# Optimization experiments

Measured on AMD Instinct MI355X. Metric: run time of the kernel, lower is better.

## Reference

```python
import jax, jax.numpy as jnp
import numpy as np

B, T, H, N_CLASSES = 2048, 128, 64, 32
N_STEPS = 10  # euler micro-steps over t in [0,1], step_size=0.1


def setup_inputs() -> dict:
    key = jax.random.key(0)
    ks = jax.random.split(key, 16)
    s = lambda fan_in: 1.0 / np.sqrt(fan_in)
    inp = {
        "times": jax.random.uniform(ks[0], (B, T), jnp.float32),
        "marks": jax.random.randint(ks[1], (B, T, 1), 0, N_CLASSES),
        "mask": jnp.ones((B, T), jnp.float32),
        # Diffeq.net: MLP(H+1 -> H -> H -> H), Tanh activations, Tanh final
        "W0": jax.random.uniform(ks[2], (H, H + 1), jnp.float32, -s(H + 1), s(H + 1)),
        "b0": jax.random.uniform(ks[3], (H,), jnp.float32, -s(H + 1), s(H + 1)),
        "W1": jax.random.uniform(ks[4], (H, H), jnp.float32, -s(H), s(H)),
        "b1": jax.random.uniform(ks[5], (H,), jnp.float32, -s(H), s(H)),
        "W2": jax.random.uniform(ks[6], (H, H), jnp.float32, -s(H), s(H)),
        "b2": jax.random.uniform(ks[7], (H,), jnp.float32, -s(H), s(H)),
        # Diffeq.intensity: Linear(H -> 1) + Softplus
        "Wi": jax.random.uniform(ks[8], (1, H), jnp.float32, -s(H), s(H)),
        "bi": jax.random.uniform(ks[9], (1,), jnp.float32, -s(H), s(H)) + 0.5,
        # Embedding(n_classes, H)
        "emb": jax.random.normal(ks[10], (N_CLASSES, H), jnp.float32),
        # LSTMCell(1+H, H)
        "W_ih": jax.random.uniform(ks[11], (4 * H, 1 + H), jnp.float32, -s(H), s(H)),
        "W_hh": jax.random.uniform(ks[12], (4 * H, H), jnp.float32, -s(H), s(H)),
        "b_ih": jax.random.uniform(ks[13], (4 * H,), jnp.float32, -s(H), s(H)),
        "b_hh": jax.random.uniform(ks[14], (4 * H,), jnp.float32, -s(H), s(H)),
    }
    return inp


def reference(times, marks, mask, W0, b0, W1, b1, W2, b2, Wi, bi, emb,
              W_ih, W_hh, b_ih, b_hh):
    dt = jnp.float32(1.0 / N_STEPS)

    def mlp(x):  # Diffeq.net
        x = jnp.tanh(x @ W0.T + b0)
        x = jnp.tanh(x @ W1.T + b1)
        return jnp.tanh(x @ W2.T + b2)

    def intensity(h):  # Diffeq.intensity (Softplus head) -> (B,1)
        return jax.nn.softplus(h @ Wi.T + bi)

    # faithful to original: marks[:, 1] is used at every timestep
    m1 = emb[marks[:, 1, 0]]  # (B,H)

    def step(carry, t_col):
        h, c = carry                       # (B,H), (B,H)
        t = t_col[:, None]                 # (B,1) -- diff (event time)
        # fixed-step euler solve of the Diffeq over s in [0,1]
        def euler(state, s):
            hh, integ = state
            s_t = (s * dt) * t             # (B,1) integration time scaled
            d_h = mlp(jnp.concatenate([s_t, hh], -1)) * t
            d_i = intensity(hh) * t
            return (hh + dt * d_h, integ + dt * d_i), None
        (h_ode, integ), _ = jax.lax.scan(
            euler, (h, jnp.zeros_like(t)),
            jnp.arange(N_STEPS, dtype=times.dtype))
        inten = intensity(h_ode)           # (B,1)
        # LSTMCell update with input [t, mark_embedding]
        x_in = jnp.concatenate([t, m1], -1)           # (B,1+H)
        gates = x_in @ W_ih.T + b_ih + h_ode @ W_hh.T + b_hh
        i_g, f_g, g_g, o_g = jnp.split(gates, 4, -1)
        c_new = jax.nn.sigmoid(f_g) * c + jax.nn.sigmoid(i_g) * jnp.tanh(g_g)
        h_new = jax.nn.sigmoid(o_g) * jnp.tanh(c_new)
        nll = (-jnp.log(inten) + integ)[:, 0]          # (B,)
        return (h_new, c_new), (h_ode, nll)

    h0 = jnp.zeros((times.shape[0], emb.shape[1]), times.dtype)
    _, (hidden, nll) = jax.lax.scan(step, (h0, h0), times.T)
    hidden = jnp.transpose(hidden, (1, 0, 2))   # (B,T,H)
    nll = nll.T                                  # (B,T)
    loss = (nll * mask).sum() / mask.sum()
    return loss, hidden
```

## Files before the change

### kernel.cpp

```cpp
#include <hip/hip_runtime.h>


#define T_LEN 128

typedef float  f32x4  __attribute__((ext_vector_type(4)));
typedef __bf16 bf16x8 __attribute__((ext_vector_type(8)));
typedef __bf16 bf16x2 __attribute__((ext_vector_type(2)));

#define MFMA16(a, b, c) __builtin_amdgcn_mfma_f32_16x16x32_bf16((a), (b), (c), 0, 0, 0)

__device__ __forceinline__ float rcp_f(float x) { return __builtin_amdgcn_rcpf(x); }
__device__ __forceinline__ float exp2_f(float x) { return __builtin_amdgcn_exp2f(x); }
__device__ __forceinline__ float log2_f(float x) { return __builtin_amdgcn_logf(x); }

__device__ __forceinline__ void bar_lds() {
  asm volatile("s_waitcnt lgkmcnt(0)" ::: "memory");
  __builtin_amdgcn_s_barrier();
  __builtin_amdgcn_sched_barrier(0);
}

constexpr float kL2E = 1.44269504088896340736f;
constexpr float kLN2 = 0.69314718055994530942f;

__device__ __forceinline__ float tanh_fast(float x) {
  float e = exp2_f(x * (2.0f * kL2E));
  return 1.0f - 2.0f * rcp_f(e + 1.0f);
}
__device__ __forceinline__ float sigm_fast(float x) {
  return rcp_f(1.0f + exp2_f(-kL2E * x));
}
__device__ __forceinline__ float softplus_fast(float x) {
  float neg = log2_f(1.0f + exp2_f(-kL2E * fabsf(x))) * kLN2;
  return fmaxf(x, 0.0f) + neg;
}
__device__ __forceinline__ unsigned packbf(float a, float b) {
  bf16x2 v; v[0] = (__bf16)a; v[1] = (__bf16)b;
  return __builtin_bit_cast(unsigned, v);
}

__launch_bounds__(256)
__global__ void jumpode_main(
    const float* __restrict__ times, const int* __restrict__ marks,
    const float* __restrict__ maskp, const float* __restrict__ W0,
    const float* __restrict__ b0,    const float* __restrict__ W1,
    const float* __restrict__ b1,    const float* __restrict__ W2,
    const float* __restrict__ b2,    const float* __restrict__ Wi,
    const float* __restrict__ bi,    const float* __restrict__ emb,
    const float* __restrict__ W_ih,  const float* __restrict__ W_hh,
    const float* __restrict__ b_ih,  const float* __restrict__ b_hh,
    float* __restrict__ out, float* __restrict__ ws)
{
  __shared__ __align__(16) unsigned whh_l[256 * 32];
  __shared__ __align__(16) float    gm1_l[8 * 256];
  __shared__ __align__(16) unsigned xb0[16 * 32];
  __shared__ __align__(16) unsigned xb1[16 * 32];
  __shared__ __align__(16) unsigned xb2[16 * 32];
  __shared__ __align__(16) float    pint[3][160];
  __shared__ __align__(16) float    b0_l[64], b1_l[64], b2_l[64];
  __shared__ __align__(16) float    w0c0_l[64];
  __shared__ __align__(16) float    wihc0_l[256];
  __shared__ __align__(16) float    emb16[8][64];
  __shared__ __align__(16) float    tim_l[8][T_LEN];
  __shared__ __align__(16) float    msk_l[8][T_LEN];

  const int tid = threadIdx.x;
  const int wv  = tid >> 6;
  const int l   = tid & 63;
  const int b   = l & 15;
  const int q   = l >> 4;
  const int bm  = b & 7;
  const int row = blockIdx.x * 8 + bm;
  const int xsw = bm;

  if (tid < 64) {
    b0_l[tid] = b0[tid]; b1_l[tid] = b1[tid]; b2_l[tid] = b2[tid];
    w0c0_l[tid] = W0[tid * 65];
  }
  wihc0_l[tid] = W_ih[tid * 65];
  for (int idx = tid; idx < 512; idx += 256) {
    int rr = idx >> 6, cc = idx & 63;
    int mk = marks[(blockIdx.x * 8 + rr) * T_LEN + 1];
    emb16[rr][cc] = emb[mk * 64 + cc];
  }
  for (int idx = tid; idx < 1024; idx += 256) {
    int rr = idx >> 7, cc = idx & 127;
    tim_l[rr][cc] = times[(blockIdx.x * 8 + rr) * T_LEN + cc];
    msk_l[rr][cc] = maskp[(blockIdx.x * 8 + rr) * T_LEN + cc];
  }
  #pragma unroll 4
  for (int i = 0; i < 32; ++i) {
    int idx = i * 256 + tid;
    int rw = idx >> 5, c2 = idx & 31;
    unsigned pw = packbf(W_hh[rw * 64 + 2 * c2], W_hh[rw * 64 + 2 * c2 + 1]);
    int gr = c2 >> 2;
    whh_l[rw * 32 + ((gr ^ (rw & 7)) << 2) + (c2 & 3)] = pw;
  }
  __syncthreads();

  {
    int g = tid;
    float acc[8];
    #pragma unroll
    for (int bb = 0; bb < 8; ++bb) acc[bb] = 0.0f;
    const float* wr = &W_ih[g * 65 + 1];
    for (int k = 0; k < 64; ++k) {
      float w = wr[k];
      #pragma unroll
      for (int bb = 0; bb < 8; ++bb) acc[bb] += w * emb16[bb][k];
    }
    float bias = b_ih[g] + b_hh[g];
    int gg = g >> 2;
    #pragma unroll
    for (int bb = 0; bb < 8; ++bb)
      gm1_l[bb * 256 + ((gg ^ bb) << 2) + (g & 3)] = acc[bb] + bias;
  }

  bf16x8 w0f[2], w1f[2], w2f[2];
  {
    const int fm = 16 * wv + b;
    #pragma unroll
    for (int kt = 0; kt < 2; ++kt) {
      const float* r0 = &W0[fm * 65 + 1 + kt * 32 + q * 8];
      const float* r1 = &W1[fm * 64 +     kt * 32 + q * 8];
      const float* r2 = &W2[fm * 64 +     kt * 32 + q * 8];
      bf16x8 a, bb, c;
      #pragma unroll
      for (int e = 0; e < 8; ++e) {
        a[e] = (__bf16)r0[e]; bb[e] = (__bf16)r1[e]; c[e] = (__bf16)r2[e];
      }
      w0f[kt] = a; w1f[kt] = bb; w2f[kt] = c;
    }
  }
  f32x4 wiv;
  #pragma unroll
  for (int r = 0; r < 4; ++r) wiv[r] = Wi[16 * wv + 4 * q + r];
  const float bi_s = bi[0];
  const f32x4 b0v = *(const f32x4*)&b0_l[16 * wv + 4 * q];
  const f32x4 b1v = *(const f32x4*)&b1_l[16 * wv + 4 * q];
  const f32x4 b2v = *(const f32x4*)&b2_l[16 * wv + 4 * q];
  const f32x4 c0v = *(const f32x4*)&w0c0_l[16 * wv + 4 * q];
  const f32x4 zf  = (f32x4){0.f, 0.f, 0.f, 0.f};
  __syncthreads();

  auto write_x = [&](unsigned* buf, const f32x4 v) {
    if (b < 8) {
      int gr = (2 * wv + (q >> 1)) ^ xsw;
      int wb = b * 32 + (gr << 2) + ((q & 1) << 1);
      buf[wb]     = packbf(v[0], v[1]);
      buf[wb + 1] = packbf(v[2], v[3]);
    }
  };
  auto read_bfrag = [&](const unsigned* buf, int kt) -> bf16x8 {
    int gr = (kt * 4 + q) ^ xsw;
    return *(const bf16x8*)((const char*)buf + bm * 128 + gr * 16);
  };
  auto whh_frag = [&](int R, int kt) -> bf16x8 {
    int rw = R * 16 + b;
    int gr = (kt * 4 + q) ^ (b & 7);
    return *(const bf16x8*)((const char*)whh_l + rw * 128 + gr * 16);
  };
  auto ld_gm1 = [&](int R) -> f32x4 {
    int gr = (R * 4 + q) ^ bm;
    return *(const f32x4*)((const char*)gm1_l + bm * 1024 + gr * 16);
  };
  auto isect_partial = [&](float* pb, const f32x4 v) {
    float part = wiv[0] * v[0] + wiv[1] * v[1] + wiv[2] * v[2] + wiv[3] * v[3];
    if (b < 8) pb[b * 20 + wv * 4 + q] = part;
  };
  auto isect_sum = [&](const float* pb) -> float {
    const char* base = (const char*)pb + bm * 80;
    f32x4 p0 = *(const f32x4*)(base);
    f32x4 p1 = *(const f32x4*)(base + 16);
    f32x4 p2 = *(const f32x4*)(base + 32);
    f32x4 p3 = *(const f32x4*)(base + 48);
    f32x4 s = p0 + p1 + p2 + p3;
    return s[0] + s[1] + s[2] + s[3];
  };

  f32x4 hst = zf, cst = zf;
  float nll_acc = 0.f, m_acc = 0.f;
  const float sel0 = (wv == 0 && q == 0 && b < 8) ? 1.0f : 0.0f;

  f32x4 hh, cin1;
  float integ, dtt, st, tb;

  auto euler_substep = [&](unsigned* BA, unsigned* BB, float* PB) {
    isect_partial(PB, hh);
    write_x(BA, hh);
    bar_lds();
    bf16x8 Bf0 = read_bfrag(BA, 0), Bf1 = read_bfrag(BA, 1);

    f32x4 a0 = MFMA16(w0f[0], Bf0, cin1);
    f32x4 a1 = MFMA16(w0f[1], Bf1, zf);
    integ += dtt * softplus_fast(isect_sum(PB) + bi_s);
    f32x4 y;
    #pragma unroll
    for (int r = 0; r < 4; ++r) y[r] = tanh_fast(a0[r] + a1[r]);
    write_x(BB, y);
    bar_lds();
    Bf0 = read_bfrag(BB, 0); Bf1 = read_bfrag(BB, 1);

    a0 = MFMA16(w1f[0], Bf0, b1v);
    a1 = MFMA16(w1f[1], Bf1, zf);
    #pragma unroll
    for (int r = 0; r < 4; ++r) y[r] = tanh_fast(a0[r] + a1[r]);
    write_x(BA, y);
    bar_lds();
    Bf0 = read_bfrag(BA, 0); Bf1 = read_bfrag(BA, 1);

    a0 = MFMA16(w2f[0], Bf0, b2v);
    a1 = MFMA16(w2f[1], Bf1, zf);
    st += dtt;
    #pragma unroll
    for (int r = 0; r < 4; ++r) cin1[r] = b0v[r] + c0v[r] * st;
    #pragma unroll
    for (int r = 0; r < 4; ++r) hh[r] += dtt * tanh_fast(a0[r] + a1[r]);
  };

  #pragma unroll 1
  for (int step = 0; step < T_LEN; ++step) {
    tb  = tim_l[bm][step];
    dtt = 0.1f * tb;
    hh  = hst;
    integ = 0.f;
    st  = 0.f;
    cin1 = b0v;

    f32x4 gcin[4];
    #pragma unroll
    for (int g = 0; g < 4; ++g) {
      const int Rb = 4 * g + wv;
      f32x4 gm = ld_gm1(Rb);
      f32x4 wc = *(const f32x4*)&wihc0_l[Rb * 16 + q * 4];
      #pragma unroll
      for (int r = 0; r < 4; ++r) gcin[g][r] = gm[r] + wc[r] * tb;
    }

    #pragma unroll 1
    for (int s2 = 0; s2 < 5; ++s2) {
      euler_substep(xb0, xb1, pint[0]);
      euler_substep(xb1, xb0, pint[1]);
    }

    bf16x8 wf[4][2];
    #pragma unroll
    for (int g = 0; g < 4; ++g) {
      wf[g][0] = whh_frag(4 * g + wv, 0);
      wf[g][1] = whh_frag(4 * g + wv, 1);
    }
    isect_partial(pint[2], hh);
    write_x(xb2, hh);
    if (b < 8) {
      size_t obase = 1 + (((size_t)row) * T_LEN + step) * 64 + 16 * wv + 4 * q;
      out[obase + 0] = hh[0]; out[obase + 1] = hh[1];
      out[obase + 2] = hh[2]; out[obase + 3] = hh[3];
    }
    bar_lds();
    bf16x8 Bf0 = read_bfrag(xb2, 0), Bf1 = read_bfrag(xb2, 1);

    f32x4 ga[4];
    #pragma unroll
    for (int g = 0; g < 4; ++g) {
      f32x4 a = MFMA16(wf[g][0], Bf0, gcin[g]);
      ga[g] = MFMA16(wf[g][1], Bf1, a);
    }
    {
      float inten = softplus_fast(isect_sum(pint[2]) + bi_s);
      float nll = -(log2_f(inten) * kLN2) + integ;
      float mval = msk_l[bm][step];
      nll_acc += sel0 * mval * nll;
      m_acc   += sel0 * mval;
    }
    #pragma unroll
    for (int r = 0; r < 4; ++r) {
      float ig = sigm_fast(ga[0][r]), fg = sigm_fast(ga[1][r]);
      float gg = tanh_fast(ga[2][r]), og = sigm_fast(ga[3][r]);
      float cn = fg * cst[r] + ig * gg;
      cst[r] = cn;
      hst[r] = og * tanh_fast(cn);
    }
  }

  if (wv == 0) {
    #pragma unroll
    for (int off = 1; off < 64; off <<= 1) {
      nll_acc += __shfl_xor(nll_acc, off);
      m_acc   += __shfl_xor(m_acc, off);
    }
    if (tid == 0) {
      atomicAdd(&ws[0], nll_acc);
      atomicAdd(&ws[1], m_acc);
    }
  }
}

__global__ void jumpode_fin(const float* __restrict__ ws, float* __restrict__ out) {
  if (threadIdx.x == 0 && blockIdx.x == 0) out[0] = ws[0] / ws[1];
}

extern "C" void kernel_launch(void* const* d_in, const int* in_sizes, int n_in,
                              void* d_out, int out_size, void* d_ws, size_t ws_size,
                              hipStream_t stream) {
  (void)in_sizes; (void)n_in; (void)out_size; (void)ws_size;
  const float* times = (const float*)d_in[0];
  const int*   marks = (const int*)  d_in[1];
  const float* maskp = (const float*)d_in[2];
  const float* W0    = (const float*)d_in[3];
  const float* b0    = (const float*)d_in[4];
  const float* W1    = (const float*)d_in[5];
  const float* b1    = (const float*)d_in[6];
  const float* W2    = (const float*)d_in[7];
  const float* b2    = (const float*)d_in[8];
  const float* Wi    = (const float*)d_in[9];
  const float* bi    = (const float*)d_in[10];
  const float* emb   = (const float*)d_in[11];
  const float* W_ih  = (const float*)d_in[12];
  const float* W_hh  = (const float*)d_in[13];
  const float* b_ih  = (const float*)d_in[14];
  const float* b_hh  = (const float*)d_in[15];
  float* out = (float*)d_out;
  float* ws  = (float*)d_ws;

  (void)hipMemsetAsync(d_ws, 0, 2 * sizeof(float), stream);
  jumpode_main<<<dim3(256), dim3(256), 0, stream>>>(
      times, marks, maskp, W0, b0, W1, b1, W2, b2, Wi, bi, emb,
      W_ih, W_hh, b_ih, b_hh, out, ws);
  jumpode_fin<<<dim3(1), dim3(64), 0, stream>>>(ws, out);
}
```

Before: 909.8 us.

## Process two independent row chains per block and halve the grid

```diff
diff --git a/kernel.cpp b/kernel.cpp
--- a/kernel.cpp
+++ b/kernel.cpp
@@ -51,17 +51,17 @@
     float* __restrict__ out, float* __restrict__ ws)
 {
   __shared__ __align__(16) unsigned whh_l[256 * 32];
-  __shared__ __align__(16) float    gm1_l[8 * 256];
+  __shared__ __align__(16) float    gm1_l[16 * 256];
   __shared__ __align__(16) unsigned xb0[16 * 32];
   __shared__ __align__(16) unsigned xb1[16 * 32];
   __shared__ __align__(16) unsigned xb2[16 * 32];
-  __shared__ __align__(16) float    pint[3][160];
+  __shared__ __align__(16) float    pint[3][320];
   __shared__ __align__(16) float    b0_l[64], b1_l[64], b2_l[64];
   __shared__ __align__(16) float    w0c0_l[64];
   __shared__ __align__(16) float    wihc0_l[256];
-  __shared__ __align__(16) float    emb16[8][64];
-  __shared__ __align__(16) float    tim_l[8][T_LEN];
-  __shared__ __align__(16) float    msk_l[8][T_LEN];
+  __shared__ __align__(16) float    emb16[16][64];
+  __shared__ __align__(16) float    tim_l[16][T_LEN];
+  __shared__ __align__(16) float    msk_l[16][T_LEN];
 
   const int tid = threadIdx.x;
   const int wv  = tid >> 6;
@@ -69,23 +69,22 @@
   const int b   = l & 15;
   const int q   = l >> 4;
   const int bm  = b & 7;
-  const int row = blockIdx.x * 8 + bm;
-  const int xsw = bm;
+  const int rowbase = blockIdx.x * 16;
 
   if (tid < 64) {
     b0_l[tid] = b0[tid]; b1_l[tid] = b1[tid]; b2_l[tid] = b2[tid];
     w0c0_l[tid] = W0[tid * 65];
   }
   wihc0_l[tid] = W_ih[tid * 65];
-  for (int idx = tid; idx < 512; idx += 256) {
+  for (int idx = tid; idx < 1024; idx += 256) {
     int rr = idx >> 6, cc = idx & 63;
-    int mk = marks[(blockIdx.x * 8 + rr) * T_LEN + 1];
+    int mk = marks[(rowbase + rr) * T_LEN + 1];
     emb16[rr][cc] = emb[mk * 64 + cc];
   }
-  for (int idx = tid; idx < 1024; idx += 256) {
+  for (int idx = tid; idx < 2048; idx += 256) {
     int rr = idx >> 7, cc = idx & 127;
-    tim_l[rr][cc] = times[(blockIdx.x * 8 + rr) * T_LEN + cc];
-    msk_l[rr][cc] = maskp[(blockIdx.x * 8 + rr) * T_LEN + cc];
+    tim_l[rr][cc] = times[(rowbase + rr) * T_LEN + cc];
+    msk_l[rr][cc] = maskp[(rowbase + rr) * T_LEN + cc];
   }
   #pragma unroll 4
   for (int i = 0; i < 32; ++i) {
@@ -99,20 +98,20 @@
 
   {
     int g = tid;
-    float acc[8];
-    #pragma unroll
-    for (int bb = 0; bb < 8; ++bb) acc[bb] = 0.0f;
+    float acc[16];
+    #pragma unroll
+    for (int bb = 0; bb < 16; ++bb) acc[bb] = 0.0f;
     const float* wr = &W_ih[g * 65 + 1];
     for (int k = 0; k < 64; ++k) {
       float w = wr[k];
       #pragma unroll
-      for (int bb = 0; bb < 8; ++bb) acc[bb] += w * emb16[bb][k];
+      for (int bb = 0; bb < 16; ++bb) acc[bb] += w * emb16[bb][k];
     }
     float bias = b_ih[g] + b_hh[g];
     int gg = g >> 2;
     #pragma unroll
-    for (int bb = 0; bb < 8; ++bb)
-      gm1_l[bb * 256 + ((gg ^ bb) << 2) + (g & 3)] = acc[bb] + bias;
+    for (int bb = 0; bb < 16; ++bb)
+      gm1_l[bb * 256 + ((gg ^ (bb & 7)) << 2) + (g & 3)] = acc[bb] + bias;
   }
 
   bf16x8 w0f[2], w1f[2], w2f[2];
@@ -142,33 +141,38 @@
   const f32x4 zf  = (f32x4){0.f, 0.f, 0.f, 0.f};
   __syncthreads();
 
-  auto write_x = [&](unsigned* buf, const f32x4 v) {
-    if (b < 8) {
-      int gr = (2 * wv + (q >> 1)) ^ xsw;
-      int wb = b * 32 + (gr << 2) + ((q & 1) << 1);
-      buf[wb]     = packbf(v[0], v[1]);
-      buf[wb + 1] = packbf(v[2], v[3]);
-    }
-  };
-  auto read_bfrag = [&](const unsigned* buf, int kt) -> bf16x8 {
-    int gr = (kt * 4 + q) ^ xsw;
-    return *(const bf16x8*)((const char*)buf + bm * 128 + gr * 16);
+  auto write_x = [&](unsigned* buf, const f32x4 vA, const f32x4 vB) {
+    f32x4 v;
+    #pragma unroll
+    for (int r = 0; r < 4; ++r) v[r] = (b < 8) ? vA[r] : vB[r];
+    int gr = (2 * wv + (q >> 1)) ^ bm;
+    int wb = b * 32 + (gr << 2) + ((q & 1) << 1);
+    buf[wb]     = packbf(v[0], v[1]);
+    buf[wb + 1] = packbf(v[2], v[3]);
+  };
+  auto read_bfrag = [&](const unsigned* buf, int kt, int chain) -> bf16x8 {
+    int col = bm + 8 * chain;
+    int gr = (kt * 4 + q) ^ bm;
+    return *(const bf16x8*)((const char*)buf + col * 128 + gr * 16);
   };
   auto whh_frag = [&](int R, int kt) -> bf16x8 {
     int rw = R * 16 + b;
     int gr = (kt * 4 + q) ^ (b & 7);
     return *(const bf16x8*)((const char*)whh_l + rw * 128 + gr * 16);
   };
-  auto ld_gm1 = [&](int R) -> f32x4 {
-    int gr = (R * 4 + q) ^ bm;
-    return *(const f32x4*)((const char*)gm1_l + bm * 1024 + gr * 16);
-  };
-  auto isect_partial = [&](float* pb, const f32x4 v) {
+  auto ld_gm1 = [&](int row, int R) -> f32x4 {
+    int gr = (R * 4 + q) ^ (row & 7);
+    return *(const f32x4*)((const char*)gm1_l + row * 1024 + gr * 16);
+  };
+  auto isect_partial = [&](float* pb, const f32x4 vA, const f32x4 vB) {
+    f32x4 v;
+    #pragma unroll
+    for (int r = 0; r < 4; ++r) v[r] = (b < 8) ? vA[r] : vB[r];
     float part = wiv[0] * v[0] + wiv[1] * v[1] + wiv[2] * v[2] + wiv[3] * v[3];
-    if (b < 8) pb[b * 20 + wv * 4 + q] = part;
+    pb[b * 20 + wv * 4 + q] = part;
   };
   auto isect_sum = [&](const float* pb) -> float {
-    const char* base = (const char*)pb + bm * 80;
+    const char* base = (const char*)pb + b * 80;
     f32x4 p0 = *(const f32x4*)(base);
     f32x4 p1 = *(const f32x4*)(base + 16);
     f32x4 p2 = *(const f32x4*)(base + 32);
@@ -177,64 +181,77 @@
     return s[0] + s[1] + s[2] + s[3];
   };
 
-  f32x4 hst = zf, cst = zf;
+  f32x4 hstA = zf, cstA = zf, hstB = zf, cstB = zf;
   float nll_acc = 0.f, m_acc = 0.f;
-  const float sel0 = (wv == 0 && q == 0 && b < 8) ? 1.0f : 0.0f;
-
-  f32x4 hh, cin1;
-  float integ, dtt, st, tb;
+  const float sel = (wv == 0 && q == 0) ? 1.0f : 0.0f;
+
+  f32x4 hhA, hhB, cin1A, cin1B;
+  float integ_own, dttA, dttB, dtt_own, stA, stB, tbA, tbB;
 
   auto euler_substep = [&](unsigned* BA, unsigned* BB, float* PB) {
-    isect_partial(PB, hh);
-    write_x(BA, hh);
+    isect_partial(PB, hhA, hhB);
+    write_x(BA, hhA, hhB);
     bar_lds();
-    bf16x8 Bf0 = read_bfrag(BA, 0), Bf1 = read_bfrag(BA, 1);
-
-    f32x4 a0 = MFMA16(w0f[0], Bf0, cin1);
-    f32x4 a1 = MFMA16(w0f[1], Bf1, zf);
-    integ += dtt * softplus_fast(isect_sum(PB) + bi_s);
-    f32x4 y;
-    #pragma unroll
-    for (int r = 0; r < 4; ++r) y[r] = tanh_fast(a0[r] + a1[r]);
-    write_x(BB, y);
+    bf16x8 A0 = read_bfrag(BA, 0, 0), A1 = read_bfrag(BA, 1, 0);
+    bf16x8 B0 = read_bfrag(BA, 0, 1), B1 = read_bfrag(BA, 1, 1);
+
+    f32x4 aA0 = MFMA16(w0f[0], A0, cin1A);
+    f32x4 aA1 = MFMA16(w0f[1], A1, zf);
+    f32x4 aB0 = MFMA16(w0f[0], B0, cin1B);
+    f32x4 aB1 = MFMA16(w0f[1], B1, zf);
+    integ_own += dtt_own * softplus_fast(isect_sum(PB) + bi_s);
+    f32x4 yA, yB;
+    #pragma unroll
+    for (int r = 0; r < 4; ++r) {
+      yA[r] = tanh_fast(aA0[r] + aA1[r]);
+      yB[r] = tanh_fast(aB0[r] + aB1[r]);
+    }
+    write_x(BB, yA, yB);
     bar_lds();
-    Bf0 = read_bfrag(BB, 0); Bf1 = read_bfrag(BB, 1);
-
-    a0 = MFMA16(w1f[0], Bf0, b1v);
-    a1 = MFMA16(w1f[1], Bf1, zf);
-    #pragma unroll
-    for (int r = 0; r < 4; ++r) y[r] = tanh_fast(a0[r] + a1[r]);
-    write_x(BA, y);
+    A0 = read_bfrag(BB, 0, 0); A1 = read_bfrag(BB, 1, 0);
+    B0 = read_bfrag(BB, 0, 1); B1 = read_bfrag(BB, 1, 1);
+
+    aA0 = MFMA16(w1f[0], A0, b1v);
+    aA1 = MFMA16(w1f[1], A1, zf);
+    aB0 = MFMA16(w1f[0], B0, b1v);
+    aB1 = MFMA16(w1f[1], B1, zf);
+    #pragma unroll
+    for (int r = 0; r < 4; ++r) {
+      yA[r] = tanh_fast(aA0[r] + aA1[r]);
+      yB[r] = tanh_fast(aB0[r] + aB1[r]);
+    }
+    write_x(BA, yA, yB);
     bar_lds();
-    Bf0 = read_bfrag(BA, 0); Bf1 = read_bfrag(BA, 1);
-
-    a0 = MFMA16(w2f[0], Bf0, b2v);
-    a1 = MFMA16(w2f[1], Bf1, zf);
-    st += dtt;
-    #pragma unroll
-    for (int r = 0; r < 4; ++r) cin1[r] = b0v[r] + c0v[r] * st;
-    #pragma unroll
-    for (int r = 0; r < 4; ++r) hh[r] += dtt * tanh_fast(a0[r] + a1[r]);
+    A0 = read_bfrag(BA, 0, 0); A1 = read_bfrag(BA, 1, 0);
+    B0 = read_bfrag(BA, 0, 1); B1 = read_bfrag(BA, 1, 1);
+
+    aA0 = MFMA16(w2f[0], A0, b2v);
+    aA1 = MFMA16(w2f[1], A1, zf);
+    aB0 = MFMA16(w2f[0], B0, b2v);
+    aB1 = MFMA16(w2f[1], B1, zf);
+    stA += dttA; stB += dttB;
+    #pragma unroll
+    for (int r = 0; r < 4; ++r) {
+      cin1A[r] = b0v[r] + c0v[r] * stA;
+      cin1B[r] = b0v[r] + c0v[r] * stB;
+    }
+    #pragma unroll
+    for (int r = 0; r < 4; ++r) {
+      hhA[r] += dttA * tanh_fast(aA0[r] + aA1[r]);
+      hhB[r] += dttB * tanh_fast(aB0[r] + aB1[r]);
+    }
   };
 
   #pragma unroll 1
   for (int step = 0; step < T_LEN; ++step) {
-    tb  = tim_l[bm][step];
-    dtt = 0.1f * tb;
-    hh  = hst;
-    integ = 0.f;
-    st  = 0.f;
-    cin1 = b0v;
-
-    f32x4 gcin[4];
-    #pragma unroll
-    for (int g = 0; g < 4; ++g) {
-      const int Rb = 4 * g + wv;
-      f32x4 gm = ld_gm1(Rb);
-      f32x4 wc = *(const f32x4*)&wihc0_l[Rb * 16 + q * 4];
-      #pragma unroll
-      for (int r = 0; r < 4; ++r) gcin[g][r] = gm[r] + wc[r] * tb;
-    }
+    tbA = tim_l[bm][step];
+    tbB = tim_l[8 + bm][step];
+    dttA = 0.1f * tbA; dttB = 0.1f * tbB;
+    dtt_own = (b < 8) ? dttA : dttB;
+    hhA = hstA; hhB = hstB;
+    integ_own = 0.f;
+    stA = 0.f; stB = 0.f;
+    cin1A = b0v; cin1B = b0v;
 
     #pragma unroll 1
     for (int s2 = 0; s2 < 5; ++s2) {
@@ -243,41 +260,65 @@
     }
 
     bf16x8 wf[4][2];
+    f32x4 gcA[4], gcB[4];
     #pragma unroll
     for (int g = 0; g < 4; ++g) {
-      wf[g][0] = whh_frag(4 * g + wv, 0);
-      wf[g][1] = whh_frag(4 * g + wv, 1);
-    }
-    isect_partial(pint[2], hh);
-    write_x(xb2, hh);
-    if (b < 8) {
-      size_t obase = 1 + (((size_t)row) * T_LEN + step) * 64 + 16 * wv + 4 * q;
-      out[obase + 0] = hh[0]; out[obase + 1] = hh[1];
-      out[obase + 2] = hh[2]; out[obase + 3] = hh[3];
+      const int Rb = 4 * g + wv;
+      wf[g][0] = whh_frag(Rb, 0);
+      wf[g][1] = whh_frag(Rb, 1);
+      f32x4 wc = *(const f32x4*)&wihc0_l[Rb * 16 + q * 4];
+      f32x4 gA = ld_gm1(bm, Rb), gB = ld_gm1(8 + bm, Rb);
+      #pragma unroll
+      for (int r = 0; r < 4; ++r) {
+        gcA[g][r] = gA[r] + wc[r] * tbA;
+        gcB[g][r] = gB[r] + wc[r] * tbB;
+      }
+    }
+    isect_partial(pint[2], hhA, hhB);
+    write_x(xb2, hhA, hhB);
+    {
+      f32x4 vo;
+      #pragma unroll
+      for (int r = 0; r < 4; ++r) vo[r] = (b < 8) ? hhA[r] : hhB[r];
+      size_t obase = 1 + (((size_t)(rowbase + b)) * T_LEN + step) * 64
+                       + 16 * wv + 4 * q;
+      out[obase + 0] = vo[0]; out[obase + 1] = vo[1];
+      out[obase + 2] = vo[2]; out[obase + 3] = vo[3];
     }
     bar_lds();
-    bf16x8 Bf0 = read_bfrag(xb2, 0), Bf1 = read_bfrag(xb2, 1);
-
-    f32x4 ga[4];
+    bf16x8 A0 = read_bfrag(xb2, 0, 0), A1 = read_bfrag(xb2, 1, 0);
+    bf16x8 B0 = read_bfrag(xb2, 0, 1), B1 = read_bfrag(xb2, 1, 1);
+
+    f32x4 gaA[4], gaB[4];
     #pragma unroll
     for (int g = 0; g < 4; ++g) {
-      f32x4 a = MFMA16(wf[g][0], Bf0, gcin[g]);
-      ga[g] = MFMA16(wf[g][1], Bf1, a);
+      f32x4 a = MFMA16(wf[g][0], A0, gcA[g]);
+      gaA[g] = MFMA16(wf[g][1], A1, a);
+      f32x4 a2 = MFMA16(wf[g][0], B0, gcB[g]);
+      gaB[g] = MFMA16(wf[g][1], B1, a2);
     }
     {
       float inten = softplus_fast(isect_sum(pint[2]) + bi_s);
-      float nll = -(log2_f(inten) * kLN2) + integ;
-      float mval = msk_l[bm][step];
-      nll_acc += sel0 * mval * nll;
-      m_acc   += sel0 * mval;
-    }
-    #pragma unroll
-    for (int r = 0; r < 4; ++r) {
-      float ig = sigm_fast(ga[0][r]), fg = sigm_fast(ga[1][r]);
-      float gg = tanh_fast(ga[2][r]), og = sigm_fast(ga[3][r]);
-      float cn = fg * cst[r] + ig * gg;
-      cst[r] = cn;
-      hst[r] = og * tanh_fast(cn);
+      float nll = -(log2_f(inten) * kLN2) + integ_own;
+      float mval = msk_l[b][step];
+      nll_acc += sel * mval * nll;
+      m_acc   += sel * mval;
+    }
+    #pragma unroll
+    for (int r = 0; r < 4; ++r) {
+      float ig = sigm_fast(gaA[0][r]), fg = sigm_fast(gaA[1][r]);
+      float gg = tanh_fast(gaA[2][r]), og = sigm_fast(gaA[3][r]);
+      float cn = fg * cstA[r] + ig * gg;
+      cstA[r] = cn;
+      hstA[r] = og * tanh_fast(cn);
+    }
+    #pragma unroll
+    for (int r = 0; r < 4; ++r) {
+      float ig = sigm_fast(gaB[0][r]), fg = sigm_fast(gaB[1][r]);
+      float gg = tanh_fast(gaB[2][r]), og = sigm_fast(gaB[3][r]);
+      float cn = fg * cstB[r] + ig * gg;
+      cstB[r] = cn;
+      hstB[r] = og * tanh_fast(cn);
     }
   }
 
@@ -322,7 +363,7 @@
   float* ws  = (float*)d_ws;
 
   (void)hipMemsetAsync(d_ws, 0, 2 * sizeof(float), stream);
-  jumpode_main<<<dim3(256), dim3(256), 0, stream>>>(
+  jumpode_main<<<dim3(128), dim3(256), 0, stream>>>(
       times, marks, maskp, W0, b0, W1, b1, W2, b2, Wi, bi, emb,
       W_ih, W_hh, b_ih, b_hh, out, ws);
   jumpode_fin<<<dim3(1), dim3(64), 0, stream>>>(ws, out);
```

New measurement: 1.358 ms. 49.3% more time.
